# Kernel optimization log

Measured on AMD Instinct MI355X. Metric: run time of the kernel, lower is better.

Reference implementation:

```python
import jax, jax.numpy as jnp
import numpy as np

EPS_LN = 1e-5
EPS_BN = 1e-5
NEG_SLOPE = 0.2


def gat_conv(x, src, tgt, W, a_src, a_dst, b, heads, out_ch, concat):
    """PyG-style GATConv (self loops already appended to src/tgt).
    x: (N, F_in); W: (F_in, heads*out_ch); a_src/a_dst: (heads, out_ch); b: bias."""
    N = x.shape[0]
    h = (x @ W).reshape(N, heads, out_ch)          # (N,H,C)
    alpha_src = (h * a_src).sum(-1)                # (N,H)
    alpha_dst = (h * a_dst).sum(-1)                # (N,H)
    e = jax.nn.leaky_relu(alpha_src[src] + alpha_dst[tgt], NEG_SLOPE)  # (E,H)
    # softmax over incoming edges of each target node
    m = jax.ops.segment_max(e, tgt, num_segments=N)
    e = jnp.exp(e - m[tgt])
    denom = jax.ops.segment_sum(e, tgt, num_segments=N)
    alpha = e / (denom[tgt] + 1e-16)               # (E,H)
    out = jax.ops.segment_sum(h[src] * alpha[..., None], tgt, num_segments=N)  # (N,H,C)
    out = out.reshape(N, heads * out_ch) if concat else out.mean(axis=1)
    return out + b


def conv_transpose3d(x, W, stride=2, pad=1):
    """torch ConvTranspose3d. x: (N,Cin,D,H,W); W: (Cin,Cout,k,k,k)."""
    k = W.shape[2]
    rhs = jnp.flip(W, axis=(2, 3, 4)).transpose(1, 0, 2, 3, 4)  # (Cout,Cin,k,k,k)
    return jax.lax.conv_general_dilated(
        x, rhs, window_strides=(1, 1, 1),
        padding=[(k - 1 - pad, k - 1 - pad)] * 3,
        lhs_dilation=(stride, stride, stride),
        dimension_numbers=('NCDHW', 'OIDHW', 'NCDHW'))


def setup_inputs() -> dict:
    key = jax.random.key(0)
    ks = jax.random.split(key, 16)
    N, F_IN, HID, HEADS, OUT = 48, 9, 8, 4, 9
    E = 768
    s = lambda k, shape, sc=0.1: jax.random.normal(k, shape, jnp.float32) * sc
    inp = {
        'obj_feats': jax.random.normal(ks[0], (N, F_IN), jnp.float32),
        'edge_index': jax.random.randint(ks[1], (2, E), 0, N),
        'volumes': jax.random.normal(ks[2], (N, OUT, 64, 64, 64), jnp.float32),
        # gnn1: GATConv(9 -> 8, heads=4, concat)
        'W1': s(ks[3], (F_IN, HEADS * HID), 0.3),
        'a_src1': s(ks[4], (HEADS, HID), 0.3),
        'a_dst1': s(ks[5], (HEADS, HID), 0.3),
        'b1': jnp.zeros((HEADS * HID,), jnp.float32),
        # gnn2: GATConv(32 -> 9, heads=1, mean)
        'W2': s(ks[6], (HEADS * HID, OUT), 0.2),
        'a_src2': s(ks[7], (1, OUT), 0.3),
        'a_dst2': s(ks[8], (1, OUT), 0.3),
        'b2': jnp.zeros((OUT,), jnp.float32),
        'ln_g': jnp.ones((OUT,), jnp.float32),
        'ln_b': jnp.zeros((OUT,), jnp.float32),
        'proj_scale': jnp.float32(0.5),
        'lin_W': s(ks[9], (OUT, 32 * 4 * 4 * 4), 0.2),
        'lin_b': jnp.zeros((32 * 4 * 4 * 4,), jnp.float32),
        'ct1_W': s(ks[10], (32, 16, 4, 4, 4), 0.1),
        'ct1_b': jnp.zeros((16,), jnp.float32),
        'ct2_W': s(ks[11], (16, OUT, 4, 4, 4), 0.1),
        'ct2_b': jnp.zeros((OUT,), jnp.float32),
        'bn_g': jnp.ones((OUT,), jnp.float32),
        'bn_b': jnp.zeros((OUT,), jnp.float32),
    }
    return inp


def reference(obj_feats, edge_index, volumes, W1, a_src1, a_dst1, b1,
              W2, a_src2, a_dst2, b2, ln_g, ln_b, proj_scale,
              lin_W, lin_b, ct1_W, ct1_b, ct2_W, ct2_b, bn_g, bn_b):
    N = obj_feats.shape[0]
    loops = jnp.arange(N, dtype=edge_index.dtype)
    src = jnp.concatenate([edge_index[0], loops])  # PyG add_self_loops=True
    tgt = jnp.concatenate([edge_index[1], loops])

    x = jax.nn.relu(gat_conv(obj_feats, src, tgt, W1, a_src1, a_dst1, b1, 4, 8, True))
    x = gat_conv(x, src, tgt, W2, a_src2, a_dst2, b2, 1, 9, False)
    # LayerNorm(output_dim) + residual
    mu = x.mean(-1, keepdims=True)
    var = ((x - mu) ** 2).mean(-1, keepdims=True)
    x = ln_g * (x - mu) * jax.lax.rsqrt(var + EPS_LN) + ln_b + obj_feats

    # projector: Linear -> ReLU -> (N,32,4,4,4) -> ConvT -> ReLU -> ConvT -> BatchNorm3d
    h = jax.nn.relu(x @ lin_W + lin_b).reshape(N, 32, 4, 4, 4)
    h = jax.nn.relu(conv_transpose3d(h, ct1_W) + ct1_b[:, None, None, None])
    h = conv_transpose3d(h, ct2_W) + ct2_b[:, None, None, None]     # (N,9,16,16,16)
    bm = h.mean(axis=(0, 2, 3, 4), keepdims=True)
    bv = ((h - bm) ** 2).mean(axis=(0, 2, 3, 4), keepdims=True)     # biased, training-mode BN
    proj = bn_g[:, None, None, None] * (h - bm) * jax.lax.rsqrt(bv + EPS_BN) + bn_b[:, None, None, None]

    # trilinear upsample (align_corners=False == half-pixel == jax.image default)
    proj = jax.image.resize(proj, volumes.shape, method='trilinear')
    return volumes + proj_scale * proj
```

## Files before the change

### kernel.cpp

```cpp
#include <hip/hip_runtime.h>

#define EPS_LN 1e-5f
#define EPS_BN 1e-5f

typedef float f4 __attribute__((ext_vector_type(4)));

__device__ __forceinline__ float lrelu(float v) { return v >= 0.f ? v : 0.2f * v; }

__device__ __forceinline__ void axis16(int o, int& i0, int& i1, float& f) {
  int t = 2 * o - 3;
  int q = (t >= 0) ? (t >> 3) : -1;
  f = (float)(t - 8 * q) * 0.125f;
  i0 = q < 0 ? 0 : q;
  i1 = q + 1 > 15 ? 15 : q + 1;
}

__global__ __launch_bounds__(512) void kA2(
    const float* __restrict__ obj, const int* __restrict__ eidx,
    const float* __restrict__ W1, const float* __restrict__ as1w,
    const float* __restrict__ ad1w, const float* __restrict__ b1,
    const float* __restrict__ W2, const float* __restrict__ as2w,
    const float* __restrict__ ad2w, const float* __restrict__ b2,
    const float* __restrict__ lng, const float* __restrict__ lnb,
    float* __restrict__ xlg)
{
  const int tid = threadIdx.x;
  __shared__ float xin[48][9];
  __shared__ float h1[48][32];
  __shared__ float a1s[48][4], a1d[48][4];
  __shared__ float m1[48][4], r1[48][4];
  __shared__ float w1[816][4];
  __shared__ float x2[48][32];
  __shared__ float h2s[48][9];
  __shared__ float a2s[48], a2d[48], m2[48], r2[48];
  __shared__ float w2[816];
  __shared__ float g2[48][9];
  __shared__ int esrc[816], etgt[816];
  __shared__ int es[816], et[816];
  __shared__ int chunkCnt[48][48];
  __shared__ int offs[49], colsum[48];

  for (int i = tid; i < 768; i += 512) { esrc[i] = eidx[i]; etgt[i] = eidx[768 + i]; }
  if (tid < 48) { esrc[768 + tid] = tid; etgt[768 + tid] = tid; }
  for (int i = tid; i < 432; i += 512) xin[i / 9][i % 9] = obj[i];
  for (int i = tid; i < 2304; i += 512) ((int*)chunkCnt)[i] = 0;
  __syncthreads();

  if (tid < 48) {
    const int c = tid;
    for (int j = 0; j < 17; ++j) chunkCnt[c][etgt[c * 17 + j]]++;
  }
  __syncthreads();
  if (tid < 48) {
    int s = 0;
    for (int c = 0; c < 48; ++c) s += chunkCnt[c][tid];
    colsum[tid] = s;
  }
  __syncthreads();
  if (tid == 0) { offs[0] = 0; for (int n = 0; n < 48; ++n) offs[n + 1] = offs[n] + colsum[n]; }
  __syncthreads();
  if (tid < 48) {
    int run = offs[tid];
    for (int c = 0; c < 48; ++c) { int v = chunkCnt[c][tid]; chunkCnt[c][tid] = run; run += v; }
  }
  __syncthreads();
  if (tid < 48) {
    const int c = tid;
    for (int j = 0; j < 17; ++j) {
      int e = c * 17 + j, n = etgt[e];
      int pos = chunkCnt[c][n]++;
      es[pos] = esrc[e]; et[pos] = n;
    }
  }

  for (int i = tid; i < 1536; i += 512) {
    int n = i >> 5, j = i & 31;
    float s = 0.f;
    for (int f = 0; f < 9; ++f) s += xin[n][f] * W1[f * 32 + j];
    h1[n][j] = s;
  }
  __syncthreads();

  for (int i = tid; i < 192; i += 512) {
    int n = i >> 2, h = i & 3;
    float ss = 0.f, sd = 0.f;
    for (int c = 0; c < 8; ++c) {
      float v = h1[n][h * 8 + c];
      ss += v * as1w[h * 8 + c];
      sd += v * ad1w[h * 8 + c];
    }
    a1s[n][h] = ss; a1d[n][h] = sd;
  }
  __syncthreads();

  for (int i = tid; i < 192; i += 512) {
    int n = i >> 2, h = i & 3;
    float ad = a1d[n][h];
    float mx = -1e30f;
    for (int p = offs[n]; p < offs[n + 1]; ++p)
      mx = fmaxf(mx, lrelu(a1s[es[p]][h] + ad));
    m1[n][h] = mx;
  }
  __syncthreads();

  for (int i = tid; i < 3264; i += 512) {
    int p = i >> 2, h = i & 3, n = et[p];
    w1[p][h] = expf(lrelu(a1s[es[p]][h] + a1d[n][h]) - m1[n][h]);
  }
  __syncthreads();

  for (int i = tid; i < 192; i += 512) {
    int n = i >> 2, h = i & 3;
    float s = 0.f;
    for (int p = offs[n]; p < offs[n + 1]; ++p) s += w1[p][h];
    r1[n][h] = 1.f / (s + 1e-16f);
  }
  __syncthreads();

  for (int i = tid; i < 1536; i += 512) {
    int n = i >> 5, j = i & 31, h = j >> 3;
    float acc = 0.f;
    for (int p = offs[n]; p < offs[n + 1]; ++p)
      acc += w1[p][h] * h1[es[p]][j];
    x2[n][j] = fmaxf(acc * r1[n][h] + b1[j], 0.f);
  }
  __syncthreads();

  for (int i = tid; i < 432; i += 512) {
    int n = i / 9, k = i % 9;
    float s = 0.f;
    for (int c = 0; c < 32; ++c) s += x2[n][c] * W2[c * 9 + k];
    h2s[n][k] = s;
  }
  __syncthreads();
  if (tid < 48) {
    float ss = 0.f, sd = 0.f;
    for (int k = 0; k < 9; ++k) { ss += h2s[tid][k] * as2w[k]; sd += h2s[tid][k] * ad2w[k]; }
    a2s[tid] = ss; a2d[tid] = sd;
  }
  __syncthreads();
  if (tid < 48) {
    float ad = a2d[tid];
    float mx = -1e30f;
    for (int p = offs[tid]; p < offs[tid + 1]; ++p)
      mx = fmaxf(mx, lrelu(a2s[es[p]] + ad));
    m2[tid] = mx;
  }
  __syncthreads();
  for (int i = tid; i < 816; i += 512) {
    int n = et[i];
    w2[i] = expf(lrelu(a2s[es[i]] + a2d[n]) - m2[n]);
  }
  __syncthreads();
  if (tid < 48) {
    float s = 0.f;
    for (int p = offs[tid]; p < offs[tid + 1]; ++p) s += w2[p];
    r2[tid] = 1.f / (s + 1e-16f);
  }
  __syncthreads();
  for (int i = tid; i < 432; i += 512) {
    int n = i / 9, k = i % 9;
    float acc = 0.f;
    for (int p = offs[n]; p < offs[n + 1]; ++p)
      acc += w2[p] * h2s[es[p]][k];
    g2[n][k] = acc * r2[n] + b2[k];
  }
  __syncthreads();

  if (tid < 48) {
    float mu = 0.f;
    for (int k = 0; k < 9; ++k) mu += g2[tid][k];
    mu *= (1.f / 9.f);
    float var = 0.f;
    for (int k = 0; k < 9; ++k) { float dd = g2[tid][k] - mu; var += dd * dd; }
    var *= (1.f / 9.f);
    float is = rsqrtf(var + EPS_LN);
    for (int k = 0; k < 9; ++k)
      xlg[tid * 9 + k] = lng[k] * (g2[tid][k] - mu) * is + lnb[k] + xin[tid][k];
  }
}

__global__ __launch_bounds__(256) void kBC(
    const float* __restrict__ xlg, const float* __restrict__ linW,
    const float* __restrict__ linb, const float* __restrict__ w,
    const float* __restrict__ bias, float* __restrict__ outp)
{
  const int co = blockIdx.x, n = blockIdx.y, tid = threadIdx.x;
  __shared__ float xls[9];
  __shared__ float xs[2048];
  __shared__ float wsd[2048];
  if (tid < 9) xls[tid] = xlg[n * 9 + tid];
  for (int q = tid; q < 2048; q += 256) {
    int ci = q >> 6, t = q & 63;
    wsd[q] = w[ci * 1024 + co * 64 + t];
  }
  __syncthreads();
  for (int q = tid; q < 2048; q += 256) {
    float s = linb[q];
#pragma unroll
    for (int k = 0; k < 9; ++k) s += xls[k] * linW[k * 2048 + q];
    xs[q] = fmaxf(s, 0.f);
  }
  __syncthreads();

  const int od = tid >> 5, oh = (tid >> 2) & 7, owp = tid & 3;
  float acc0 = 0.f, acc1 = 0.f;
  const int kd0 = 1 - (od & 1), kh0 = 1 - (oh & 1);
#pragma unroll
  for (int kdi = 0; kdi < 2; ++kdi) {
    int kd = kd0 + 2 * kdi;
    int id = (od + 1 - kd) >> 1;
    if ((unsigned)id >= 4u) continue;
#pragma unroll
    for (int khi = 0; khi < 2; ++khi) {
      int kh = kh0 + 2 * khi;
      int ih = (oh + 1 - kh) >> 1;
      if ((unsigned)ih >= 4u) continue;
      for (int ci = 0; ci < 32; ++ci) {
        const float* xr = &xs[ci * 64 + id * 16 + ih * 4];
        const float* wr = &wsd[ci * 64 + kd * 16 + kh * 4];
        float x0 = xr[owp];
        float xm1 = owp > 0 ? xr[owp - 1] : 0.f;
        float xp1 = owp < 3 ? xr[owp + 1] : 0.f;
        acc0 += x0 * wr[1];
        acc0 += xm1 * wr[3];
        acc1 += xp1 * wr[0];
        acc1 += x0 * wr[2];
      }
    }
  }
  const float bb = bias[co];
  float2 o;
  o.x = fmaxf(acc0 + bb, 0.f);
  o.y = fmaxf(acc1 + bb, 0.f);
  *(float2*)&outp[(n * 16 + co) * 512 + od * 64 + oh * 8 + 2 * owp] = o;
}

__global__ __launch_bounds__(256) void kD(
    const float* __restrict__ x, const float* __restrict__ w,
    const float* __restrict__ bias, float* __restrict__ outp,
    float* __restrict__ psum, float* __restrict__ pssq)
{
  const int co = blockIdx.x, n = blockIdx.y, tid = threadIdx.x;
  __shared__ float xs[8192];
  __shared__ float wsd[1024];
  __shared__ float rs[256], rq[256];
  {
    const float4* src = (const float4*)(x + (size_t)n * 8192);
    float4* dst = (float4*)xs;
    for (int q = tid; q < 2048; q += 256) dst[q] = src[q];
  }
  for (int q = tid; q < 1024; q += 256) {
    int ci = q >> 6, t = q & 63;
    wsd[q] = w[(ci * 9 + co) * 64 + t];
  }
  __syncthreads();
  const int od = tid >> 4, oh = tid & 15;
  float acc[16];
#pragma unroll
  for (int i = 0; i < 16; ++i) acc[i] = 0.f;
  const int kd0 = 1 - (od & 1), kh0 = 1 - (oh & 1);
#pragma unroll
  for (int kdi = 0; kdi < 2; ++kdi) {
    int kd = kd0 + 2 * kdi;
    int id = (od + 1 - kd) >> 1;
    if ((unsigned)id >= 8u) continue;
#pragma unroll
    for (int khi = 0; khi < 2; ++khi) {
      int kh = kh0 + 2 * khi;
      int ih = (oh + 1 - kh) >> 1;
      if ((unsigned)ih >= 8u) continue;
      for (int ci = 0; ci < 16; ++ci) {
        const float* xr = &xs[ci * 512 + id * 64 + ih * 8];
        const float* wr = &wsd[ci * 64 + kd * 16 + kh * 4];
        float xv[8], wv[4];
#pragma unroll
        for (int t = 0; t < 8; ++t) xv[t] = xr[t];
#pragma unroll
        for (int t = 0; t < 4; ++t) wv[t] = wr[t];
#pragma unroll
        for (int ow = 0; ow < 16; ++ow) {
          const int kw0 = 1 - (ow & 1);
          const int iw0 = (ow + 1 - kw0) >> 1;
          if (iw0 < 8) acc[ow] += xv[iw0] * wv[kw0];
          if (iw0 - 1 >= 0) acc[ow] += xv[iw0 - 1] * wv[kw0 + 2];
        }
      }
    }
  }
  const float bb = bias[co];
  float s = 0.f, q = 0.f;
  float4* op = (float4*)(outp + (size_t)(n * 9 + co) * 4096 + od * 256 + oh * 16);
#pragma unroll
  for (int t = 0; t < 4; ++t) {
    float4 v;
    v.x = acc[4 * t] + bb; v.y = acc[4 * t + 1] + bb;
    v.z = acc[4 * t + 2] + bb; v.w = acc[4 * t + 3] + bb;
    op[t] = v;
    s += v.x + v.y + v.z + v.w;
    q += v.x * v.x + v.y * v.y + v.z * v.z + v.w * v.w;
  }
  rs[tid] = s; rq[tid] = q;
  __syncthreads();
  for (int off = 128; off > 0; off >>= 1) {
    if (tid < off) { rs[tid] += rs[tid + off]; rq[tid] += rq[tid + off]; }
    __syncthreads();
  }
  if (tid == 0) { psum[co * 48 + n] = rs[0]; pssq[co * 48 + n] = rq[0]; }
}

__global__ __launch_bounds__(256) void kF6(
    const float* __restrict__ vol, const float* __restrict__ h2,
    const float* __restrict__ psum, const float* __restrict__ pssq,
    const float* __restrict__ bng, const float* __restrict__ bnb,
    const float* __restrict__ scp, float* __restrict__ outp)
{
  const int slab = blockIdx.x, c = blockIdx.y, n = blockIdx.z, tid = threadIdx.x;
  __shared__ float hs[768];
  __shared__ float plane[4096];
  __shared__ float abS[2];

  const int od_base = slab * 4;
  const size_t gbase = ((size_t)(n * 9 + c) * 64 + od_base) * 1024;
  const f4* v4 = (const f4*)vol;
  f4* o4 = (f4*)outp;

  f4 vv0[8];
#pragma unroll
  for (int i = 0; i < 8; ++i) vv0[i] = v4[gbase + (size_t)(tid + i * 256)];

  int zb = slab - 1;
  zb = zb < 0 ? 0 : (zb > 13 ? 13 : zb);
  if (tid < 192) {
    const f4* src = (const f4*)(h2 + (size_t)(n * 9 + c) * 4096) + zb * 64;
    ((f4*)hs)[tid] = src[tid];
  }
  if (tid < 64) {
    float s = (tid < 48) ? psum[c * 48 + tid] : 0.f;
    float q = (tid < 48) ? pssq[c * 48 + tid] : 0.f;
#pragma unroll
    for (int off = 32; off > 0; off >>= 1) {
      s += __shfl_down(s, off);
      q += __shfl_down(q, off);
    }
    if (tid == 0) {
      float mean = s * (1.f / 196608.f);
      float var = q * (1.f / 196608.f) - mean * mean;
      float Aa = bng[c] * rsqrtf(var + EPS_BN);
      abS[0] = Aa;
      abS[1] = bnb[c] - Aa * mean;
    }
  }
  const float sc = scp[0];
  __syncthreads();

#pragma unroll
  for (int j = 0; j < 16; ++j) {
    int e = tid + j * 256;
    int x = e & 15, oh = (e >> 4) & 63, od = e >> 10;
    int z0, z1, y0, y1; float fz, fy;
    axis16(od_base + od, z0, z1, fz);
    axis16(oh, y0, y1, fy);
    float w00 = (1.f - fz) * (1.f - fy), w01 = (1.f - fz) * fy;
    float w10 = fz * (1.f - fy), w11 = fz * fy;
    int bz0 = (z0 - zb) << 8, bz1 = (z1 - zb) << 8;
    int by0 = y0 << 4, by1 = y1 << 4;
    plane[e] = w00 * hs[bz0 + by0 + x] + w01 * hs[bz0 + by1 + x]
             + w10 * hs[bz1 + by0 + x] + w11 * hs[bz1 + by1 + x];
  }
  __syncthreads();

  f4 vv1[8];
#pragma unroll
  for (int i = 0; i < 8; ++i) vv1[i] = v4[gbase + (size_t)(tid + (8 + i) * 256)];

  const float Aa = abS[0], Bb = abS[1];

#pragma unroll
  for (int i = 0; i < 8; ++i) {
    int u = tid + i * 256;
    int owq = u & 15, base = (u >> 4) << 4;
    int xa = owq ? owq - 1 : 0;
    int xc = owq < 15 ? owq + 1 : 15;
    float A = plane[base + xa], B = plane[base + owq], C = plane[base + xc];
    f4 oo;
    oo.x = vv0[i].x + sc * fmaf(Aa, A + 0.625f * (B - A), Bb);
    oo.y = vv0[i].y + sc * fmaf(Aa, A + 0.875f * (B - A), Bb);
    oo.z = vv0[i].z + sc * fmaf(Aa, B + 0.125f * (C - B), Bb);
    oo.w = vv0[i].w + sc * fmaf(Aa, B + 0.375f * (C - B), Bb);
    o4[gbase + (size_t)u] = oo;
  }
#pragma unroll
  for (int i = 0; i < 8; ++i) {
    int u = tid + (8 + i) * 256;
    int owq = u & 15, base = (u >> 4) << 4;
    int xa = owq ? owq - 1 : 0;
    int xc = owq < 15 ? owq + 1 : 15;
    float A = plane[base + xa], B = plane[base + owq], C = plane[base + xc];
    f4 oo;
    oo.x = vv1[i].x + sc * fmaf(Aa, A + 0.625f * (B - A), Bb);
    oo.y = vv1[i].y + sc * fmaf(Aa, A + 0.875f * (B - A), Bb);
    oo.z = vv1[i].z + sc * fmaf(Aa, B + 0.125f * (C - B), Bb);
    oo.w = vv1[i].w + sc * fmaf(Aa, B + 0.375f * (C - B), Bb);
    o4[gbase + (size_t)u] = oo;
  }
}

extern "C" void kernel_launch(void* const* d_in, const int* in_sizes, int n_in,
                              void* d_out, int out_size, void* d_ws, size_t ws_size,
                              hipStream_t stream) {
  (void)in_sizes; (void)n_in; (void)out_size; (void)ws_size;
  const float* obj  = (const float*)d_in[0];
  const int*   eidx = (const int*)d_in[1];
  const float* vol  = (const float*)d_in[2];
  const float* W1   = (const float*)d_in[3];
  const float* as1  = (const float*)d_in[4];
  const float* ad1  = (const float*)d_in[5];
  const float* b1   = (const float*)d_in[6];
  const float* W2   = (const float*)d_in[7];
  const float* as2  = (const float*)d_in[8];
  const float* ad2  = (const float*)d_in[9];
  const float* b2   = (const float*)d_in[10];
  const float* lng  = (const float*)d_in[11];
  const float* lnb  = (const float*)d_in[12];
  const float* scp  = (const float*)d_in[13];
  const float* linW = (const float*)d_in[14];
  const float* linb = (const float*)d_in[15];
  const float* ct1W = (const float*)d_in[16];
  const float* ct1b = (const float*)d_in[17];
  const float* ct2W = (const float*)d_in[18];
  const float* ct2b = (const float*)d_in[19];
  const float* bng  = (const float*)d_in[20];
  const float* bnb  = (const float*)d_in[21];

  float* ws   = (float*)d_ws;
  float* xlg  = ws;
  float* hct1 = ws + 432;
  float* h2   = ws + 393648;
  float* psum = ws + 2163120;
  float* pssq = ws + 2163552;

  float* out = (float*)d_out;

  kA2<<<1, 512, 0, stream>>>(obj, eidx, W1, as1, ad1, b1, W2, as2, ad2, b2,
                             lng, lnb, xlg);
  kBC<<<dim3(16, 48), 256, 0, stream>>>(xlg, linW, linb, ct1W, ct1b, hct1);
  kD<<<dim3(9, 48), 256, 0, stream>>>(hct1, ct2W, ct2b, h2, psum, pssq);
  kF6<<<dim3(16, 9, 48), 256, 0, stream>>>(vol, h2, psum, pssq, bng, bnb, scp, out);
}
```

Before: 249.5 us.

## Split BN finalize into tiny kernel and flatten upsample to one-vec4-per-thread

The batch-norm statistics reduction moves out of every upsample block into a separate single-block kernel that writes the per-channel scale and shift. The upsample/add kernel is rewritten so each thread handles one float4 of output. The z/y interpolation is read directly from global (L2-cached) h2, and the x-neighbour values come from wavefront shuffles instead of a shared-memory plane. This removes the shared-memory staging, the two barriers and the repeated per-block stats reduction, at the cost of an extra launch, more redundant gathers from h2, and less memory-level parallelism per thread.

```diff
diff --git a/kernel.cpp b/kernel.cpp
--- a/kernel.cpp
+++ b/kernel.cpp
@@ -309,101 +309,58 @@
   if (tid == 0) { psum[co * 48 + n] = rs[0]; pssq[co * 48 + n] = rq[0]; }
 }
 
-__global__ __launch_bounds__(256) void kF6(
-    const float* __restrict__ vol, const float* __restrict__ h2,
+__global__ __launch_bounds__(64) void kE2(
     const float* __restrict__ psum, const float* __restrict__ pssq,
     const float* __restrict__ bng, const float* __restrict__ bnb,
-    const float* __restrict__ scp, float* __restrict__ outp)
+    float* __restrict__ AB)
 {
-  const int slab = blockIdx.x, c = blockIdx.y, n = blockIdx.z, tid = threadIdx.x;
-  __shared__ float hs[768];
-  __shared__ float plane[4096];
-  __shared__ float abS[2];
-
-  const int od_base = slab * 4;
-  const size_t gbase = ((size_t)(n * 9 + c) * 64 + od_base) * 1024;
-  const f4* v4 = (const f4*)vol;
-  f4* o4 = (f4*)outp;
-
-  f4 vv0[8];
-#pragma unroll
-  for (int i = 0; i < 8; ++i) vv0[i] = v4[gbase + (size_t)(tid + i * 256)];
-
-  int zb = slab - 1;
-  zb = zb < 0 ? 0 : (zb > 13 ? 13 : zb);
-  if (tid < 192) {
-    const f4* src = (const f4*)(h2 + (size_t)(n * 9 + c) * 4096) + zb * 64;
-    ((f4*)hs)[tid] = src[tid];
-  }
-  if (tid < 64) {
-    float s = (tid < 48) ? psum[c * 48 + tid] : 0.f;
-    float q = (tid < 48) ? pssq[c * 48 + tid] : 0.f;
-#pragma unroll
-    for (int off = 32; off > 0; off >>= 1) {
-      s += __shfl_down(s, off);
-      q += __shfl_down(q, off);
-    }
-    if (tid == 0) {
-      float mean = s * (1.f / 196608.f);
-      float var = q * (1.f / 196608.f) - mean * mean;
-      float Aa = bng[c] * rsqrtf(var + EPS_BN);
-      abS[0] = Aa;
-      abS[1] = bnb[c] - Aa * mean;
-    }
-  }
-  const float sc = scp[0];
-  __syncthreads();
-
-#pragma unroll
-  for (int j = 0; j < 16; ++j) {
-    int e = tid + j * 256;
-    int x = e & 15, oh = (e >> 4) & 63, od = e >> 10;
-    int z0, z1, y0, y1; float fz, fy;
-    axis16(od_base + od, z0, z1, fz);
-    axis16(oh, y0, y1, fy);
-    float w00 = (1.f - fz) * (1.f - fy), w01 = (1.f - fz) * fy;
-    float w10 = fz * (1.f - fy), w11 = fz * fy;
-    int bz0 = (z0 - zb) << 8, bz1 = (z1 - zb) << 8;
-    int by0 = y0 << 4, by1 = y1 << 4;
-    plane[e] = w00 * hs[bz0 + by0 + x] + w01 * hs[bz0 + by1 + x]
-             + w10 * hs[bz1 + by0 + x] + w11 * hs[bz1 + by1 + x];
-  }
-  __syncthreads();
-
-  f4 vv1[8];
-#pragma unroll
-  for (int i = 0; i < 8; ++i) vv1[i] = v4[gbase + (size_t)(tid + (8 + i) * 256)];
-
-  const float Aa = abS[0], Bb = abS[1];
-
-#pragma unroll
-  for (int i = 0; i < 8; ++i) {
-    int u = tid + i * 256;
-    int owq = u & 15, base = (u >> 4) << 4;
-    int xa = owq ? owq - 1 : 0;
-    int xc = owq < 15 ? owq + 1 : 15;
-    float A = plane[base + xa], B = plane[base + owq], C = plane[base + xc];
-    f4 oo;
-    oo.x = vv0[i].x + sc * fmaf(Aa, A + 0.625f * (B - A), Bb);
-    oo.y = vv0[i].y + sc * fmaf(Aa, A + 0.875f * (B - A), Bb);
-    oo.z = vv0[i].z + sc * fmaf(Aa, B + 0.125f * (C - B), Bb);
-    oo.w = vv0[i].w + sc * fmaf(Aa, B + 0.375f * (C - B), Bb);
-    o4[gbase + (size_t)u] = oo;
-  }
-#pragma unroll
-  for (int i = 0; i < 8; ++i) {
-    int u = tid + (8 + i) * 256;
-    int owq = u & 15, base = (u >> 4) << 4;
-    int xa = owq ? owq - 1 : 0;
-    int xc = owq < 15 ? owq + 1 : 15;
-    float A = plane[base + xa], B = plane[base + owq], C = plane[base + xc];
-    f4 oo;
-    oo.x = vv1[i].x + sc * fmaf(Aa, A + 0.625f * (B - A), Bb);
-    oo.y = vv1[i].y + sc * fmaf(Aa, A + 0.875f * (B - A), Bb);
-    oo.z = vv1[i].z + sc * fmaf(Aa, B + 0.125f * (C - B), Bb);
-    oo.w = vv1[i].w + sc * fmaf(Aa, B + 0.375f * (C - B), Bb);
-    o4[gbase + (size_t)u] = oo;
-  }
+  const int c = threadIdx.x;
+  if (c >= 9) return;
+  float s = 0.f, q = 0.f;
+  for (int n = 0; n < 48; ++n) { s += psum[c * 48 + n]; q += pssq[c * 48 + n]; }
+  float mean = s * (1.f / 196608.f);
+  float var = q * (1.f / 196608.f) - mean * mean;
+  float Aa = bng[c] * rsqrtf(var + EPS_BN);
+  AB[c] = Aa;
+  AB[9 + c] = bnb[c] - Aa * mean;
+}
+
+__global__ __launch_bounds__(256) void kF7(
+    const float* __restrict__ vol, const float* __restrict__ h2,
+    const float* __restrict__ AB, const float* __restrict__ scp,
+    float* __restrict__ outp)
+{
+  const int g = blockIdx.x * 256 + threadIdx.x;
+  const int x = g & 15;
+  const int oh = (g >> 4) & 63;
+  const int od = (g >> 10) & 63;
+  const int nc = g >> 16;
+
+  const float* hb = h2 + (size_t)nc * 4096;
+  int z0, z1, y0, y1; float fz, fy;
+  axis16(od, z0, z1, fz);
+  axis16(oh, y0, y1, fy);
+  float w00 = (1.f - fz) * (1.f - fy), w01 = (1.f - fz) * fy;
+  float w10 = fz * (1.f - fy), w11 = fz * fy;
+  float zyv = w00 * hb[z0 * 256 + y0 * 16 + x] + w01 * hb[z0 * 256 + y1 * 16 + x]
+            + w10 * hb[z1 * 256 + y0 * 16 + x] + w11 * hb[z1 * 256 + y1 * 16 + x];
+
+  const int lane = threadIdx.x & 63;
+  const int gb = lane & 48;
+  float A = __shfl(zyv, gb | (x ? x - 1 : 0));
+  float C = __shfl(zyv, gb | (x < 15 ? x + 1 : 15));
+  float B = zyv;
+
+  const int c = nc % 9;
+  const float Aa = AB[c], Bb = AB[9 + c], sc = scp[0];
+
+  f4 vv = ((const f4*)vol)[g];
+  f4 oo;
+  oo.x = vv.x + sc * fmaf(Aa, A + 0.625f * (B - A), Bb);
+  oo.y = vv.y + sc * fmaf(Aa, A + 0.875f * (B - A), Bb);
+  oo.z = vv.z + sc * fmaf(Aa, B + 0.125f * (C - B), Bb);
+  oo.w = vv.w + sc * fmaf(Aa, B + 0.375f * (C - B), Bb);
+  ((f4*)outp)[g] = oo;
 }
 
 extern "C" void kernel_launch(void* const* d_in, const int* in_sizes, int n_in,
@@ -439,6 +396,7 @@
   float* h2   = ws + 393648;
   float* psum = ws + 2163120;
   float* pssq = ws + 2163552;
+  float* AB   = ws + 2163984;
 
   float* out = (float*)d_out;
 
@@ -446,5 +404,6 @@
                              lng, lnb, xlg);
   kBC<<<dim3(16, 48), 256, 0, stream>>>(xlg, linW, linb, ct1W, ct1b, hct1);
   kD<<<dim3(9, 48), 256, 0, stream>>>(hct1, ct2W, ct2b, h2, psum, pssq);
-  kF6<<<dim3(16, 9, 48), 256, 0, stream>>>(vol, h2, psum, pssq, bng, bnb, scp, out);
-}
+  kE2<<<1, 64, 0, stream>>>(psum, pssq, bng, bnb, AB);
+  kF7<<<110592, 256, 0, stream>>>(vol, h2, AB, scp, out);
+}
```

Result: faster. 226.9 us (-9.0%).
